# Kernel optimization log

Hardware: AMD Instinct MI355X
Metric: run time of the kernel (lower is better)

Reference implementation:

```python
import jax, jax.numpy as jnp
import numpy as np

B, T, I, H = 32, 8192, 16, 128
G = 3 * H  # gru gate dim
LN_EPS = 1e-5


def _ln(v):
    # LayerNorm over last dim, elementwise_affine=False
    m = jnp.mean(v, axis=-1, keepdims=True)
    var = jnp.mean(jnp.square(v - m), axis=-1, keepdims=True)
    return (v - m) * jax.lax.rsqrt(var + LN_EPS)


def setup_inputs() -> dict:
    key = jax.random.key(0)
    ks = jax.random.split(key, 10)
    std = 1.0 / np.sqrt(H)
    u = lambda k, shape: jax.random.uniform(k, shape, jnp.float32, -std, std)
    return {
        "xs": jax.random.normal(ks[0], (B, T, I), jnp.float32),
        "state": jax.random.normal(ks[1], (1, B, H), jnp.float32),
        "alpha_i": jax.random.normal(ks[2], (B, G), jnp.float32),
        "beta_i": jax.random.normal(ks[3], (B, G), jnp.float32),
        "alpha_h": jax.random.normal(ks[4], (B, G), jnp.float32),
        "beta_h": jax.random.normal(ks[5], (B, G), jnp.float32),
        "Wx": u(ks[6], (G, I)),
        "bx": u(ks[7], (G,)),
        "Wh": u(ks[8], (G, H)),
        "bh": u(ks[9], (G,)),
    }


def reference(xs, state, alpha_i, beta_i, alpha_h, beta_h, Wx, bx, Wh, bh):
    h0 = state[0]  # [B, H]  (rearrange '1 b h -> b 1 h' then squeeze the step dim)
    # Input projection + LayerNorm + FiLM is independent of the recurrence -> batch over T.
    ih_all = _ln(jnp.einsum('bti,gi->btg', xs, Wx) + bx)
    ih_all = ih_all * alpha_i[:, None, :] + beta_i[:, None, :]  # [B, T, 3H]

    def step(h, ih):
        hh = _ln(h @ Wh.T + bh) * alpha_h + beta_h  # [B, 3H]
        i_r, i_i, i_n = jnp.split(ih, 3, axis=-1)
        h_r, h_i, h_n = jnp.split(hh, 3, axis=-1)
        resetgate = jax.nn.sigmoid(i_r + h_r)
        inputgate = jax.nn.sigmoid(i_i + h_i)
        newgate = jnp.tanh(i_n + resetgate * h_n)
        hy = newgate + inputgate * (h - newgate)
        return hy, hy

    hT, ys = jax.lax.scan(step, h0, jnp.swapaxes(ih_all, 0, 1))  # scan over T
    outputs = jnp.swapaxes(ys, 0, 1)  # [B, T, H]
    return outputs, hT[:, None, :]  # state as [B, 1, H] like the torch module
```

## Files before the change

kernel.cpp:

```cpp
#include <hip/hip_runtime.h>


#define T_STEPS 8192
#define BATCH   32
#define HDIM    128
#define GDIM    384
#define IDIM    16
#define LN_EPS  1e-5f

typedef float f32x2 __attribute__((ext_vector_type(2)));
typedef float f32x4 __attribute__((ext_vector_type(4)));

__device__ __forceinline__ void block_barrier() {
  asm volatile("s_waitcnt lgkmcnt(0)\n\ts_barrier" ::: "memory");
}

__device__ __forceinline__ float fast_sigmoid(float x) {
  return 1.f / (1.f + __expf(-x));
}
__device__ __forceinline__ float fast_tanh(float x) {
  float e2 = __expf(2.f * x);
  return 1.f - 2.f / (e2 + 1.f);
}
__device__ __forceinline__ float hsum4(f32x4 v) {
  return (v.x + v.y) + (v.z + v.w);
}

template <int CTRL>
__device__ __forceinline__ float dppadd(float x) {
  return x + __int_as_float(
      __builtin_amdgcn_update_dpp(0, __float_as_int(x), CTRL, 0xF, 0xF, true));
}
__device__ __forceinline__ float dpp_sum16(float x) {
  x = dppadd<0xB1>(x);
  x = dppadd<0x4E>(x);
  x = dppadd<0x141>(x);
  x = dppadd<0x140>(x);
  return x;
}
__device__ __forceinline__ f32x4 wave_sum(f32x4 v) {
  v.x = dpp_sum16(v.x); v.y = dpp_sum16(v.y);
  v.z = dpp_sum16(v.z); v.w = dpp_sum16(v.w);
  v.x += __shfl_xor(v.x, 16); v.y += __shfl_xor(v.y, 16);
  v.z += __shfl_xor(v.z, 16); v.w += __shfl_xor(v.w, 16);
  v.x += __shfl_xor(v.x, 32); v.y += __shfl_xor(v.y, 32);
  v.z += __shfl_xor(v.z, 32); v.w += __shfl_xor(v.w, 32);
  return v;
}

__global__ __launch_bounds__(256, 1) void gru_one(
    const float* __restrict__ xs,
    const float* __restrict__ state,
    const float* __restrict__ alpha_i,
    const float* __restrict__ beta_i,
    const float* __restrict__ alpha_h,
    const float* __restrict__ beta_h,
    const float* __restrict__ Wx,
    const float* __restrict__ bx,
    const float* __restrict__ Wh,
    const float* __restrict__ bh,
    float* __restrict__ out)
{
  __shared__ float lds_h[HDIM];
  __shared__ __align__(16) f32x4 lds_pA[256];
  __shared__ __align__(16) f32x2 lds_pB[256];
  __shared__ __align__(16) f32x4 lds_stat[4];

  const int b    = blockIdx.x;
  const int t_   = threadIdx.x;
  const int j    = t_ & 127;
  const int half = t_ >> 7;
  const int lane = t_ & 63;
  const int wv   = t_ >> 6;

  const int rowR = j, rowI = j + HDIM, rowN = j + 2 * HDIM;

  f32x4 wr[16], wi[16], wn[16];
  {
    const f32x4* pr = (const f32x4*)(Wh + (size_t)rowR * HDIM + half * 64);
    const f32x4* pi = (const f32x4*)(Wh + (size_t)rowI * HDIM + half * 64);
    const f32x4* pn = (const f32x4*)(Wh + (size_t)rowN * HDIM + half * 64);
#pragma unroll
    for (int q = 0; q < 16; ++q) { wr[q] = pr[q]; wi[q] = pi[q]; wn[q] = pn[q]; }
  }
  f32x4 wxr[2], wxi[2], wxn[2];
  {
    const f32x4* pr = (const f32x4*)(Wx + (size_t)rowR * IDIM + half * 8);
    const f32x4* pi = (const f32x4*)(Wx + (size_t)rowI * IDIM + half * 8);
    const f32x4* pn = (const f32x4*)(Wx + (size_t)rowN * IDIM + half * 8);
#pragma unroll
    for (int q = 0; q < 2; ++q) { wxr[q] = pr[q]; wxi[q] = pi[q]; wxn[q] = pn[q]; }
  }
#pragma unroll
  for (int q = 0; q < 16; ++q)
    asm volatile("" : "+v"(wr[q]), "+v"(wi[q]), "+v"(wn[q]));
#pragma unroll
  for (int q = 0; q < 2; ++q)
    asm volatile("" : "+v"(wxr[q]), "+v"(wxi[q]), "+v"(wxn[q]));

  const float bh_r = bh[rowR], bh_i = bh[rowI], bh_n = bh[rowN];
  const float bx_r = bx[rowR], bx_i = bx[rowI], bx_n = bx[rowN];
  const float ah_r = alpha_h[b * GDIM + rowR];
  const float ah_i = alpha_h[b * GDIM + rowI];
  const float ah_n = alpha_h[b * GDIM + rowN];
  const float bt_r = beta_h[b * GDIM + rowR];
  const float bt_i = beta_h[b * GDIM + rowI];
  const float bt_n = beta_h[b * GDIM + rowN];
  const float ai_r = alpha_i[b * GDIM + rowR];
  const float ai_i = alpha_i[b * GDIM + rowI];
  const float ai_n = alpha_i[b * GDIM + rowN];
  const float bi_r = beta_i[b * GDIM + rowR];
  const float bi_i = beta_i[b * GDIM + rowI];
  const float bi_n = beta_i[b * GDIM + rowN];

  float hreg = state[b * HDIM + j];
  if (t_ < HDIM) lds_h[j] = hreg;

  const f32x4* xp = (const f32x4*)(xs + (size_t)b * T_STEPS * IDIM);
  float* out_b = out + (size_t)b * T_STEPS * HDIM;

  f32x4 xA0 = xp[half * 2],     xA1 = xp[half * 2 + 1];
  f32x4 xB0 = xp[4 + half * 2], xB1 = xp[4 + half * 2 + 1];

  const float invd = 1.f / (2.f * (float)GDIM);

#define STEP(tcur, X0, X1)                                                     \
  do {                                                                         \
    block_barrier();                                       \
    const f32x4* hb = ((const f32x4*)lds_h) + half * 16;                       \
    f32x4 pr0 = {0.f, 0.f, 0.f, 0.f}, pr1 = pr0;                               \
    f32x4 pi0 = pr0, pi1 = pr0, pn0 = pr0, pn1 = pr0;                          \
    _Pragma("unroll") for (int q = 0; q < 16; q += 2) {                        \
      f32x4 h0 = hb[q], h1 = hb[q + 1];                                        \
      pr0 = __builtin_elementwise_fma(wr[q], h0, pr0);                         \
      pr1 = __builtin_elementwise_fma(wr[q + 1], h1, pr1);                     \
      pi0 = __builtin_elementwise_fma(wi[q], h0, pi0);                         \
      pi1 = __builtin_elementwise_fma(wi[q + 1], h1, pi1);                     \
      pn0 = __builtin_elementwise_fma(wn[q], h0, pn0);                         \
      pn1 = __builtin_elementwise_fma(wn[q + 1], h1, pn1);                     \
    }                                                                          \
    float accr = hsum4(pr0 + pr1);                                             \
    float acci = hsum4(pi0 + pi1);                                             \
    float accn = hsum4(pn0 + pn1);                                             \
    f32x4 qr = __builtin_elementwise_fma(                                      \
        wxr[0], X0, (f32x4){0.f, 0.f, 0.f, 0.f});                              \
    qr = __builtin_elementwise_fma(wxr[1], X1, qr);                            \
    f32x4 qi = __builtin_elementwise_fma(                                      \
        wxi[0], X0, (f32x4){0.f, 0.f, 0.f, 0.f});                              \
    qi = __builtin_elementwise_fma(wxi[1], X1, qi);                            \
    f32x4 qn = __builtin_elementwise_fma(                                      \
        wxn[0], X0, (f32x4){0.f, 0.f, 0.f, 0.f});                              \
    qn = __builtin_elementwise_fma(wxn[1], X1, qn);                            \
    float aIr = hsum4(qr), aIi = hsum4(qi), aIn = hsum4(qn);                   \
    lds_pA[t_] = (f32x4){accr, acci, accn, aIr};                               \
    lds_pB[t_] = (f32x2){aIi, aIn};                                            \
    block_barrier();                                \
    f32x4 oA = lds_pA[t_ ^ 128];                                               \
    f32x2 oB = lds_pB[t_ ^ 128];                                               \
    float Ar = accr + oA.x + bh_r;                                             \
    float Ai = acci + oA.y + bh_i;                                             \
    float An = accn + oA.z + bh_n;                                             \
    float Jr = aIr + oA.w + bx_r;                                              \
    float Ji = aIi + oB.x + bx_i;                                              \
    float Jn = aIn + oB.y + bx_n;                                              \
    f32x4 st = {Ar + Ai + An, Ar * Ar + Ai * Ai + An * An,                     \
                Jr + Ji + Jn, Jr * Jr + Ji * Ji + Jn * Jn};                    \
    st = wave_sum(st);                                                         \
    if (lane == 0) lds_stat[wv] = st;                                          \
    block_barrier();                                   \
    f32x4 sT = (lds_stat[0] + lds_stat[1]) + (lds_stat[2] + lds_stat[3]);      \
    float mH = sT.x * invd;                                                    \
    float rH = rsqrtf(sT.y * invd - mH * mH + LN_EPS);                         \
    float mI = sT.z * invd;                                                    \
    float rI = rsqrtf(sT.w * invd - mI * mI + LN_EPS);                         \
    float hhr = (Ar - mH) * rH * ah_r + bt_r;                                  \
    float hhi = (Ai - mH) * rH * ah_i + bt_i;                                  \
    float hhn = (An - mH) * rH * ah_n + bt_n;                                  \
    float ihr = (Jr - mI) * rI * ai_r + bi_r;                                  \
    float ihi = (Ji - mI) * rI * ai_i + bi_i;                                  \
    float ihn = (Jn - mI) * rI * ai_n + bi_n;                                  \
    float rg = fast_sigmoid(ihr + hhr);                                       \
    float ig = fast_sigmoid(ihi + hhi);                                       \
    float ng = fast_tanh(ihn + rg * hhn);                                     \
    float hy = ng + ig * (hreg - ng);                                          \
    hreg = hy;                                                                 \
    if (t_ < HDIM) {                                                           \
      lds_h[j] = hy;                                                           \
      out_b[(size_t)(tcur) * HDIM + j] = hy;                                   \
    }                                                                          \
    int tn = (tcur) + 2 < T_STEPS ? (tcur) + 2 : T_STEPS - 1;                  \
    X0 = xp[(size_t)tn * 4 + half * 2];                                        \
    X1 = xp[(size_t)tn * 4 + half * 2 + 1];                                    \
  } while (0)

  for (int t = 0; t < T_STEPS; t += 2) {
    STEP(t, xA0, xA1);
    STEP(t + 1, xB0, xB1);
  }
#undef STEP

  if (t_ < HDIM)
    out[(size_t)BATCH * T_STEPS * HDIM + b * HDIM + j] = hreg;
}

extern "C" void kernel_launch(void* const* d_in, const int* in_sizes, int n_in,
                              void* d_out, int out_size, void* d_ws, size_t ws_size,
                              hipStream_t stream) {
  const float* xs      = (const float*)d_in[0];
  const float* state   = (const float*)d_in[1];
  const float* alpha_i = (const float*)d_in[2];
  const float* beta_i  = (const float*)d_in[3];
  const float* alpha_h = (const float*)d_in[4];
  const float* beta_h  = (const float*)d_in[5];
  const float* Wx      = (const float*)d_in[6];
  const float* bx      = (const float*)d_in[7];
  const float* Wh      = (const float*)d_in[8];
  const float* bh      = (const float*)d_in[9];
  float* out = (float*)d_out;

  gru_one<<<dim3(BATCH), dim3(256), 0, stream>>>(
      xs, state, alpha_i, beta_i, alpha_h, beta_h, Wx, bx, Wh, bh, out);
}
```

Measured before the change: 11.71 ms.

## Split hidden-dot across 4 lane quarters with shuffle reduction, 512 threads

```diff
diff --git a/kernel.cpp b/kernel.cpp
--- a/kernel.cpp
+++ b/kernel.cpp
@@ -7,6 +7,7 @@
 #define GDIM    384
 #define IDIM    16
 #define LN_EPS  1e-5f
+#define NT      512
 
 typedef float f32x2 __attribute__((ext_vector_type(2)));
 typedef float f32x4 __attribute__((ext_vector_type(4)));
@@ -38,17 +39,15 @@
   x = dppadd<0x140>(x);
   return x;
 }
-__device__ __forceinline__ f32x4 wave_sum(f32x4 v) {
-  v.x = dpp_sum16(v.x); v.y = dpp_sum16(v.y);
-  v.z = dpp_sum16(v.z); v.w = dpp_sum16(v.w);
-  v.x += __shfl_xor(v.x, 16); v.y += __shfl_xor(v.y, 16);
-  v.z += __shfl_xor(v.z, 16); v.w += __shfl_xor(v.w, 16);
-  v.x += __shfl_xor(v.x, 32); v.y += __shfl_xor(v.y, 32);
-  v.z += __shfl_xor(v.z, 32); v.w += __shfl_xor(v.w, 32);
+__device__ __forceinline__ float qcomb(float v) {
+  v += __shfl_xor(v, 16);
+  v += __shfl_xor(v, 32);
   return v;
 }
 
-__global__ __launch_bounds__(256, 1) void gru_one(
+#define HPAD (HDIM + 12)
+
+__global__ __launch_bounds__(NT, 2) void gru_v4(
     const float* __restrict__ xs,
     const float* __restrict__ state,
     const float* __restrict__ alpha_i,
@@ -61,42 +60,33 @@
     const float* __restrict__ bh,
     float* __restrict__ out)
 {
-  __shared__ float lds_h[HDIM];
-  __shared__ __align__(16) f32x4 lds_pA[256];
-  __shared__ __align__(16) f32x2 lds_pB[256];
-  __shared__ __align__(16) f32x4 lds_stat[4];
+  __shared__ float lds_h[HPAD];
+  __shared__ __align__(16) f32x4 lds_stat[8];
 
   const int b    = blockIdx.x;
-  const int t_   = threadIdx.x;
-  const int j    = t_ & 127;
-  const int half = t_ >> 7;
-  const int lane = t_ & 63;
-  const int wv   = t_ >> 6;
+  const int tid  = threadIdx.x;
+  const int w    = tid >> 6;
+  const int lane = tid & 63;
+  const int q    = lane >> 4;
+  const int j    = w * 16 + (lane & 15);
 
   const int rowR = j, rowI = j + HDIM, rowN = j + 2 * HDIM;
 
-  f32x4 wr[16], wi[16], wn[16];
+  f32x4 wr[8], wi[8], wn[8];
   {
-    const f32x4* pr = (const f32x4*)(Wh + (size_t)rowR * HDIM + half * 64);
-    const f32x4* pi = (const f32x4*)(Wh + (size_t)rowI * HDIM + half * 64);
-    const f32x4* pn = (const f32x4*)(Wh + (size_t)rowN * HDIM + half * 64);
+    const f32x4* pr = (const f32x4*)(Wh + (size_t)rowR * HDIM + q * 32);
+    const f32x4* pi = (const f32x4*)(Wh + (size_t)rowI * HDIM + q * 32);
+    const f32x4* pn = (const f32x4*)(Wh + (size_t)rowN * HDIM + q * 32);
 #pragma unroll
-    for (int q = 0; q < 16; ++q) { wr[q] = pr[q]; wi[q] = pi[q]; wn[q] = pn[q]; }
+    for (int k = 0; k < 8; ++k) {
+      wr[k] = pr[k]; wi[k] = pi[k]; wn[k] = pn[k];
+      asm volatile("" : "+v"(wr[k]), "+v"(wi[k]), "+v"(wn[k]));
+    }
   }
-  f32x4 wxr[2], wxi[2], wxn[2];
-  {
-    const f32x4* pr = (const f32x4*)(Wx + (size_t)rowR * IDIM + half * 8);
-    const f32x4* pi = (const f32x4*)(Wx + (size_t)rowI * IDIM + half * 8);
-    const f32x4* pn = (const f32x4*)(Wx + (size_t)rowN * IDIM + half * 8);
-#pragma unroll
-    for (int q = 0; q < 2; ++q) { wxr[q] = pr[q]; wxi[q] = pi[q]; wxn[q] = pn[q]; }
-  }
-#pragma unroll
-  for (int q = 0; q < 16; ++q)
-    asm volatile("" : "+v"(wr[q]), "+v"(wi[q]), "+v"(wn[q]));
-#pragma unroll
-  for (int q = 0; q < 2; ++q)
-    asm volatile("" : "+v"(wxr[q]), "+v"(wxi[q]), "+v"(wxn[q]));
+  f32x4 wxr = ((const f32x4*)(Wx + (size_t)rowR * IDIM))[q];
+  f32x4 wxi = ((const f32x4*)(Wx + (size_t)rowI * IDIM))[q];
+  f32x4 wxn = ((const f32x4*)(Wx + (size_t)rowN * IDIM))[q];
+  asm volatile("" : "+v"(wxr), "+v"(wxi), "+v"(wxn));
 
   const float bh_r = bh[rowR], bh_i = bh[rowI], bh_n = bh[rowN];
   const float bx_r = bx[rowR], bx_i = bx[rowI], bx_n = bx[rowN];
@@ -114,61 +104,51 @@
   const float bi_n = beta_i[b * GDIM + rowN];
 
   float hreg = state[b * HDIM + j];
-  if (t_ < HDIM) lds_h[j] = hreg;
+  if (lane < 16) lds_h[j + ((j >> 5) << 2)] = hreg;
 
   const f32x4* xp = (const f32x4*)(xs + (size_t)b * T_STEPS * IDIM);
   float* out_b = out + (size_t)b * T_STEPS * HDIM;
 
-  f32x4 xA0 = xp[half * 2],     xA1 = xp[half * 2 + 1];
-  f32x4 xB0 = xp[4 + half * 2], xB1 = xp[4 + half * 2 + 1];
-
-  const float invd = 1.f / (2.f * (float)GDIM);
-
-#define STEP(tcur, X0, X1)                                                     \
+  f32x4 xA = xp[q], xB = xp[4 + q];
+
+  const float invd = 1.f / (float)GDIM;
+
+#define STEP(tcur, X)                                                          \
   do {                                                                         \
     block_barrier();                                       \
-    const f32x4* hb = ((const f32x4*)lds_h) + half * 16;                       \
-    f32x4 pr0 = {0.f, 0.f, 0.f, 0.f}, pr1 = pr0;                               \
-    f32x4 pi0 = pr0, pi1 = pr0, pn0 = pr0, pn1 = pr0;                          \
-    _Pragma("unroll") for (int q = 0; q < 16; q += 2) {                        \
-      f32x4 h0 = hb[q], h1 = hb[q + 1];                                        \
-      pr0 = __builtin_elementwise_fma(wr[q], h0, pr0);                         \
-      pr1 = __builtin_elementwise_fma(wr[q + 1], h1, pr1);                     \
-      pi0 = __builtin_elementwise_fma(wi[q], h0, pi0);                         \
-      pi1 = __builtin_elementwise_fma(wi[q + 1], h1, pi1);                     \
-      pn0 = __builtin_elementwise_fma(wn[q], h0, pn0);                         \
-      pn1 = __builtin_elementwise_fma(wn[q + 1], h1, pn1);                     \
+    const f32x4* hb = (const f32x4*)(lds_h + q * 36);                          \
+    f32x4 ar0 = {0.f, 0.f, 0.f, 0.f}, ar1 = ar0;                               \
+    f32x4 ai0 = ar0, ai1 = ar0, an0 = ar0, an1 = ar0;                          \
+    _Pragma("unroll") for (int k = 0; k < 8; k += 2) {                         \
+      f32x4 h0 = hb[k], h1 = hb[k + 1];                                        \
+      ar0 = __builtin_elementwise_fma(wr[k], h0, ar0);                         \
+      ar1 = __builtin_elementwise_fma(wr[k + 1], h1, ar1);                     \
+      ai0 = __builtin_elementwise_fma(wi[k], h0, ai0);                         \
+      ai1 = __builtin_elementwise_fma(wi[k + 1], h1, ai1);                     \
+      an0 = __builtin_elementwise_fma(wn[k], h0, an0);                         \
+      an1 = __builtin_elementwise_fma(wn[k + 1], h1, an1);                     \
     }                                                                          \
-    float accr = hsum4(pr0 + pr1);                                             \
-    float acci = hsum4(pi0 + pi1);                                             \
-    float accn = hsum4(pn0 + pn1);                                             \
-    f32x4 qr = __builtin_elementwise_fma(                                      \
-        wxr[0], X0, (f32x4){0.f, 0.f, 0.f, 0.f});                              \
-    qr = __builtin_elementwise_fma(wxr[1], X1, qr);                            \
-    f32x4 qi = __builtin_elementwise_fma(                                      \
-        wxi[0], X0, (f32x4){0.f, 0.f, 0.f, 0.f});                              \
-    qi = __builtin_elementwise_fma(wxi[1], X1, qi);                            \
-    f32x4 qn = __builtin_elementwise_fma(                                      \
-        wxn[0], X0, (f32x4){0.f, 0.f, 0.f, 0.f});                              \
-    qn = __builtin_elementwise_fma(wxn[1], X1, qn);                            \
-    float aIr = hsum4(qr), aIi = hsum4(qi), aIn = hsum4(qn);                   \
-    lds_pA[t_] = (f32x4){accr, acci, accn, aIr};                               \
-    lds_pB[t_] = (f32x2){aIi, aIn};                                            \
-    block_barrier();                                \
-    f32x4 oA = lds_pA[t_ ^ 128];                                               \
-    f32x2 oB = lds_pB[t_ ^ 128];                                               \
-    float Ar = accr + oA.x + bh_r;                                             \
-    float Ai = acci + oA.y + bh_i;                                             \
-    float An = accn + oA.z + bh_n;                                             \
-    float Jr = aIr + oA.w + bx_r;                                              \
-    float Ji = aIi + oB.x + bx_i;                                              \
-    float Jn = aIn + oB.y + bx_n;                                              \
+    float accr = hsum4(ar0 + ar1);                                             \
+    float acci = hsum4(ai0 + ai1);                                             \
+    float accn = hsum4(an0 + an1);                                             \
+    f32x4 z = {0.f, 0.f, 0.f, 0.f};                                            \
+    float aJr = hsum4(__builtin_elementwise_fma(wxr, X, z));                   \
+    float aJi = hsum4(__builtin_elementwise_fma(wxi, X, z));                   \
+    float aJn = hsum4(__builtin_elementwise_fma(wxn, X, z));                   \
+    float Ar = qcomb(accr) + bh_r;                                             \
+    float Ai = qcomb(acci) + bh_i;                                             \
+    float An = qcomb(accn) + bh_n;                                             \
+    float Jr = qcomb(aJr) + bx_r;                                              \
+    float Ji = qcomb(aJi) + bx_i;                                              \
+    float Jn = qcomb(aJn) + bx_n;                                              \
     f32x4 st = {Ar + Ai + An, Ar * Ar + Ai * Ai + An * An,                     \
                 Jr + Ji + Jn, Jr * Jr + Ji * Ji + Jn * Jn};                    \
-    st = wave_sum(st);                                                         \
-    if (lane == 0) lds_stat[wv] = st;                                          \
+    st.x = dpp_sum16(st.x); st.y = dpp_sum16(st.y);                            \
+    st.z = dpp_sum16(st.z); st.w = dpp_sum16(st.w);                            \
+    if (lane == 0) lds_stat[w] = st;                                           \
     block_barrier();                                   \
-    f32x4 sT = (lds_stat[0] + lds_stat[1]) + (lds_stat[2] + lds_stat[3]);      \
+    f32x4 sT = ((lds_stat[0] + lds_stat[1]) + (lds_stat[2] + lds_stat[3])) +   \
+               ((lds_stat[4] + lds_stat[5]) + (lds_stat[6] + lds_stat[7]));    \
     float mH = sT.x * invd;                                                    \
     float rH = rsqrtf(sT.y * invd - mH * mH + LN_EPS);                         \
     float mI = sT.z * invd;                                                    \
@@ -179,27 +159,26 @@
     float ihr = (Jr - mI) * rI * ai_r + bi_r;                                  \
     float ihi = (Ji - mI) * rI * ai_i + bi_i;                                  \
     float ihn = (Jn - mI) * rI * ai_n + bi_n;                                  \
-    float rg = fast_sigmoid(ihr + hhr);                                       \
-    float ig = fast_sigmoid(ihi + hhi);                                       \
-    float ng = fast_tanh(ihn + rg * hhn);                                     \
+    float rg = fast_sigmoid(ihr + hhr);                                        \
+    float ig = fast_sigmoid(ihi + hhi);                                        \
+    float ng = fast_tanh(ihn + rg * hhn);                                      \
     float hy = ng + ig * (hreg - ng);                                          \
     hreg = hy;                                                                 \
-    if (t_ < HDIM) {                                                           \
-      lds_h[j] = hy;                                                           \
+    if (lane < 16) {                                                           \
+      lds_h[j + ((j >> 5) << 2)] = hy;                                         \
       out_b[(size_t)(tcur) * HDIM + j] = hy;                                   \
     }                                                                          \
     int tn = (tcur) + 2 < T_STEPS ? (tcur) + 2 : T_STEPS - 1;                  \
-    X0 = xp[(size_t)tn * 4 + half * 2];                                        \
-    X1 = xp[(size_t)tn * 4 + half * 2 + 1];                                    \
+    X = xp[(size_t)tn * 4 + q];                                                \
   } while (0)
 
   for (int t = 0; t < T_STEPS; t += 2) {
-    STEP(t, xA0, xA1);
-    STEP(t + 1, xB0, xB1);
+    STEP(t, xA);
+    STEP(t + 1, xB);
   }
 #undef STEP
 
-  if (t_ < HDIM)
+  if (lane < 16)
     out[(size_t)BATCH * T_STEPS * HDIM + b * HDIM + j] = hreg;
 }
 
@@ -218,6 +197,6 @@
   const float* bh      = (const float*)d_in[9];
   float* out = (float*)d_out;
 
-  gru_one<<<dim3(BATCH), dim3(256), 0, stream>>>(
+  gru_v4<<<dim3(BATCH), dim3(NT), 0, stream>>>(
       xs, state, alpha_i, beta_i, alpha_h, beta_h, Wx, bx, Wh, bh, out);
 }
```

Measured after the change: 11.09 ms. 5.2% less time.
